# Performance work log

Measured on AMD Instinct MI355X. Metric: run time of the kernel, lower is better.

The kernel has to match this reference:

```python
import jax, jax.numpy as jnp
import numpy as np

N, K, C, G = 20000, 16, 256, 16
EPS = 1e-5


def _bn(x, p):
    # p: (4, C) stacked [gamma, beta, running_mean, running_var]; inference-mode BN
    g, b, m, v = p[0], p[1], p[2], p[3]
    return (x - m) * jax.lax.rsqrt(v + EPS) * g + b


def setup_inputs() -> dict:
    key = jax.random.key(0)
    ks = jax.random.split(key, 24)

    def w(k, shape):
        return jax.random.normal(k, shape, jnp.float32) * 0.02

    def bn_params(k, c):
        gamma = 1.0 + 0.02 * jax.random.normal(k, (c,), jnp.float32)
        return jnp.stack([gamma, jnp.zeros(c, jnp.float32), jnp.zeros(c, jnp.float32), jnp.ones(c, jnp.float32)])

    return {
        'feat': jax.random.normal(ks[0], (N, C), jnp.float32),
        'coord': jax.random.normal(ks[1], (N, 3), jnp.float32),
        'knn_indexes': jax.random.randint(ks[2], (N, K), 0, N),
        'Wq': w(ks[3], (C, C)), 'bq': w(ks[4], (C,)), 'bnq': bn_params(ks[5], C),
        'Wk': w(ks[6], (C, C)), 'bk': w(ks[7], (C,)), 'bnk': bn_params(ks[8], C),
        'Wv': w(ks[9], (C, C)), 'bv': w(ks[10], (C,)),
        'Wp1': w(ks[11], (3, C)), 'bp1': w(ks[12], (C,)), 'bnp': bn_params(ks[13], C),
        'Wp2': w(ks[14], (C, C)), 'bp2': w(ks[15], (C,)),
        'Ww1': w(ks[16], (C, G)), 'bw1': w(ks[17], (G,)), 'bnw': bn_params(ks[18], G),
        'Ww2': w(ks[19], (G, G)), 'bw2': w(ks[20], (G,)),
    }


def reference(feat, coord, knn_indexes, Wq, bq, bnq, Wk, bk, bnk, Wv, bv,
              Wp1, bp1, bnp, Wp2, bp2, Ww1, bw1, bnw, Ww2, bw2):
    # q/k: Linear -> BN -> ReLU ; v: Linear
    q = jax.nn.relu(_bn(feat @ Wq + bq, bnq))            # (n, c)
    k_all = jax.nn.relu(_bn(feat @ Wk + bk, bnk))        # (n, c)
    v_all = feat @ Wv + bv                               # (n, c)

    mask = jnp.sign(knn_indexes + 1).astype(feat.dtype)  # (n, k); -1 indices are padding
    safe_idx = jnp.clip(knn_indexes, 0, None)

    # kNN gather: padded entries map to zero rows in the torch code -> mask them here
    key_g = k_all[safe_idx] * mask[..., None]            # (n, k, c)
    value = v_all[safe_idx] * mask[..., None]            # (n, k, c)
    pos = (coord[safe_idx] - coord[:, None, :]) * mask[..., None]  # (n, k, 3)

    relation_qk = key_g - q[:, None, :]                  # (n, k, c)

    # positional-encoding bias MLP: Linear(3->c) -> BN -> ReLU -> Linear(c->c)
    peb = jax.nn.relu(_bn(pos @ Wp1 + bp1, bnp)) @ Wp2 + bp2  # (n, k, c)
    relation_qk = relation_qk + peb
    value = value + peb

    # weight encoding: Linear(c->g) -> BN -> ReLU -> Linear(g->g)
    weight = jax.nn.relu(_bn(relation_qk @ Ww1 + bw1, bnw)) @ Ww2 + bw2  # (n, k, g)
    weight = jax.nn.softmax(weight, axis=1) * mask[..., None]            # softmax over neighbors

    value = value.reshape(N, K, G, C // G)               # (n, k, g, i)
    out = jnp.einsum('nsgi,nsg->ngi', value, weight)     # group-wise weighted sum over neighbors
    return out.reshape(N, C)
```

## Files before the change

### kernel.cpp

```cpp
#include <hip/hip_runtime.h>
#include <hip/hip_bf16.h>

#define N_PTS 20000
#define KNN 16
#define C 256
#define G 16
#define EPS 1e-5f
#define NP 16

typedef __attribute__((ext_vector_type(8))) short short8;
typedef __attribute__((ext_vector_type(4))) short short4b;
typedef __attribute__((ext_vector_type(4))) float f32x4;

__device__ inline unsigned short f2bf(float f) {
    unsigned int x = __float_as_uint(f);
    unsigned int r = (x + 0x7fffu + ((x >> 16) & 1u)) >> 16;
    return (unsigned short)r;
}
__device__ inline float bf2f(unsigned int u) {
    return __uint_as_float((u & 0xffffu) << 16);
}
__device__ inline short f2bfs(float f) { return (short)f2bf(f); }

__global__ __launch_bounds__(256) void k_prep(const float* Wp2, const float* bp2,
                                              const float* Ww1, const float* bw1,
                                              float* w2w1, float* c1,
                                              unsigned short* wp2bft) {
    __shared__ float red[256][17];
    int t = threadIdx.x, b = blockIdx.x;
    float src = (b < C) ? Wp2[b * C + t] : bp2[t];
    #pragma unroll
    for (int g = 0; g < G; ++g) red[t][g] = src * Ww1[t * G + g];
    __syncthreads();
    for (int s = 128; s > 0; s >>= 1) {
        if (t < s) {
            #pragma unroll
            for (int g = 0; g < G; ++g) red[t][g] += red[t + s][g];
        }
        __syncthreads();
    }
    if (t < G) {
        if (b < C) w2w1[b * G + t] = red[0][t];
        else       c1[t] = red[0][t] + bw1[t];
    }
    if (b < C) wp2bft[t * C + b] = f2bf(Wp2[b * C + t]);
}

__global__ __launch_bounds__(512, 2) void k_qkv(
    const float* __restrict__ feat,
    const float* __restrict__ Wq, const float* __restrict__ bq, const float* __restrict__ bnq,
    const float* __restrict__ Wk, const float* __restrict__ bk, const float* __restrict__ bnk,
    const float* __restrict__ Wv, const float* __restrict__ bv,
    unsigned short* __restrict__ q_out, unsigned short* __restrict__ k_out,
    unsigned short* __restrict__ v_out) {
    __shared__ __align__(16) unsigned short Asl[128][40];
    __shared__ __align__(16) unsigned short Bsl[256][40];

    const int t = threadIdx.x;
    const int m0 = blockIdx.x * 128;
    const int z = blockIdx.z;
    const float* W    = (z == 0) ? Wq : (z == 1) ? Wk : Wv;
    const float* bias = (z == 0) ? bq : (z == 1) ? bk : bv;
    const float* bn   = (z == 0) ? bnq : bnk;

    const int wv = t >> 6, lane = t & 63, h = lane >> 4, ln = lane & 15;
    const int wm = wv >> 2, wn = wv & 3;

    f32x4 acc[4][4];
    #pragma unroll
    for (int i = 0; i < 4; ++i)
        #pragma unroll
        for (int j = 0; j < 4; ++j) acc[i][j] = (f32x4){0.f, 0.f, 0.f, 0.f};

    const int ar = t >> 3, ak = (t & 7) * 4;
    const int bk_n = (t & 63) * 4, bk_k = t >> 6;

    for (int kb = 0; kb < C; kb += 32) {
        #pragma unroll
        for (int ps = 0; ps < 2; ++ps) {
            int r = ar + 64 * ps;
            int gm = m0 + r; if (gm > N_PTS - 1) gm = N_PTS - 1;
            float4 f = *(const float4*)&feat[gm * C + kb + ak];
            unsigned int u0 = f2bf(f.x) | ((unsigned int)f2bf(f.y) << 16);
            unsigned int u1 = f2bf(f.z) | ((unsigned int)f2bf(f.w) << 16);
            *(uint2*)&Asl[r][ak] = make_uint2(u0, u1);
        }
        #pragma unroll
        for (int ps = 0; ps < 4; ++ps) {
            int kk = bk_k + 8 * ps;
            float4 w = *(const float4*)&W[(kb + kk) * C + bk_n];
            Bsl[bk_n + 0][kk] = f2bf(w.x);
            Bsl[bk_n + 1][kk] = f2bf(w.y);
            Bsl[bk_n + 2][kk] = f2bf(w.z);
            Bsl[bk_n + 3][kk] = f2bf(w.w);
        }
        __syncthreads();
        short8 af[4], bf[4];
        #pragma unroll
        for (int mf = 0; mf < 4; ++mf) af[mf] = *(const short8*)&Asl[64 * wm + 16 * mf + ln][8 * h];
        #pragma unroll
        for (int nf = 0; nf < 4; ++nf) bf[nf] = *(const short8*)&Bsl[64 * wn + 16 * nf + ln][8 * h];
        #pragma unroll
        for (int mf = 0; mf < 4; ++mf)
            #pragma unroll
            for (int nf = 0; nf < 4; ++nf)
                acc[mf][nf] = __builtin_amdgcn_mfma_f32_16x16x32_bf16(af[mf], bf[nf], acc[mf][nf], 0, 0, 0);
        __syncthreads();
    }

    unsigned short* dst = (z == 0) ? q_out : (z == 1) ? k_out : v_out;
    float scv[4], shv[4];
    int cidx[4];
    #pragma unroll
    for (int nf = 0; nf < 4; ++nf) {
        int c = 64 * wn + 16 * nf + ln;
        cidx[nf] = c;
        float bi = bias[c];
        if (z < 2) {
            float ga = bn[c], be = bn[C + c], mu = bn[2 * C + c], va = bn[3 * C + c];
            float s = ga * rsqrtf(va + EPS);
            scv[nf] = s; shv[nf] = (bi - mu) * s + be;
        } else { scv[nf] = 1.f; shv[nf] = bi; }
    }
    #pragma unroll
    for (int mf = 0; mf < 4; ++mf) {
        #pragma unroll
        for (int reg = 0; reg < 4; ++reg) {
            int m = m0 + 64 * wm + 16 * mf + 4 * h + reg;
            if (m >= N_PTS) continue;
            #pragma unroll
            for (int nf = 0; nf < 4; ++nf) {
                float x = acc[mf][nf][reg] * scv[nf] + shv[nf];
                if (z < 2) x = fmaxf(x, 0.f);
                dst[m * C + cidx[nf]] = f2bf(x);
            }
        }
    }
}

__global__ __launch_bounds__(256) void k_qkw(const unsigned short* q_ws, const unsigned short* k_ws,
                                             const float* Ww1, float* qw1, float* kw1) {
    __shared__ float tile[16][260];
    __shared__ float wT[G][260];
    int t = threadIdx.x;
    const unsigned short* src = blockIdx.y ? k_ws : q_ws;
    float* dst = blockIdx.y ? kw1 : qw1;
    int r0 = blockIdx.x * 16;
    #pragma unroll
    for (int i = 0; i < 16; ++i) {
        int e = t + 256 * i;
        wT[e & 15][e >> 4] = Ww1[e];
    }
    #pragma unroll
    for (int i = 0; i < 4; ++i) {
        int e4 = t + 256 * i;
        int row = e4 >> 6, col = (e4 & 63) * 4;
        uint2 u = *(const uint2*)&src[(r0 + row) * C + col];
        tile[row][col + 0] = bf2f(u.x);
        tile[row][col + 1] = bf2f(u.x >> 16);
        tile[row][col + 2] = bf2f(u.y);
        tile[row][col + 3] = bf2f(u.y >> 16);
    }
    __syncthreads();
    int r = t >> 4, g = t & 15;
    float acc = 0.f;
    for (int c = 0; c < C; c += 4) {
        float4 a = *(float4*)&tile[r][c];
        float4 w = *(float4*)&wT[g][c];
        acc += a.x * w.x + a.y * w.y + a.z * w.z + a.w * w.w;
    }
    dst[(r0 + r) * G + g] = acc;
}

__global__ __launch_bounds__(256, 2) void k_attn(
    const float* __restrict__ coord, const int* __restrict__ knn,
    const float* __restrict__ Wp1, const float* __restrict__ bp1, const float* __restrict__ bnp,
    const float* __restrict__ bp2,
    const float* __restrict__ Ww2, const float* __restrict__ bw2, const float* __restrict__ bnw,
    const float* __restrict__ w2w1, const float* __restrict__ c1,
    const float* __restrict__ qw1, const float* __restrict__ kw1,
    const unsigned short* __restrict__ vb, const unsigned short* __restrict__ wp2bft,
    float* __restrict__ out)
{
    __shared__ __align__(16) int   safe_s[256];
    __shared__ __align__(16) float wp1c[256][4];
    __shared__ __align__(16) unsigned short wt_l[16][16][20];
    __shared__ __align__(16) unsigned short hwbuf[10368];

    const int t = threadIdx.x;
    const int n0 = blockIdx.x * NP;
    const int wv = t >> 6, lane = t & 63, h = lane >> 4, ln = lane & 15;
    const short8 z8 = (short8){0, 0, 0, 0, 0, 0, 0, 0};

    float scwv, shwv, bw2v, c1v;
    {
        float ga = bnw[ln], be = bnw[G + ln], mu = bnw[2 * G + ln], va = bnw[3 * G + ln];
        scwv = ga * rsqrtf(va + EPS);
        shwv = be - mu * scwv;
        bw2v = bw2[ln];
        c1v  = c1[ln];
    }

    #pragma unroll
    for (int i = 0; i < 16; ++i) {
        int e = t + 256 * i;
        hwbuf[(e & 15) * 264 + (e >> 4)] = f2bf(w2w1[e]);
    }
    {
        float ga = bnp[t], be = bnp[C + t], mu = bnp[2 * C + t], va = bnp[3 * C + t];
        float s = ga * rsqrtf(va + EPS);
        wp1c[t][0] = Wp1[t] * s;
        wp1c[t][1] = Wp1[C + t] * s;
        wp1c[t][2] = Wp1[2 * C + t] * s;
        wp1c[t][3] = (bp1[t] - mu) * s + be;
        hwbuf[4224 + (t & 15) * 16 + (t >> 4)] = f2bf(Ww2[t]);
    }
    float px0, py0, pz0, mk0; int safe0;
    {
        const int n = n0 + (t >> 4);
        int ii = knn[n * KNN + (t & 15)];
        mk0 = (ii >= 0) ? 1.f : 0.f;
        safe0 = ii < 0 ? 0 : ii;
        safe_s[t] = safe0;
        px0 = (coord[safe0 * 3]     - coord[n * 3])     * mk0;
        py0 = (coord[safe0 * 3 + 1] - coord[n * 3 + 1]) * mk0;
        pz0 = (coord[safe0 * 3 + 2] - coord[n * 3 + 2]) * mk0;
    }
    __syncthreads();

    float prx[4], pry[4], prz[4];
    #pragma unroll
    for (int q = 0; q < 4; ++q) {
        int src = 16 * q + ln;
        prx[q] = __shfl(px0, src, 64);
        pry[q] = __shfl(py0, src, 64);
        prz[q] = __shfl(pz0, src, 64);
    }

    f32x4 accB[4];
    #pragma unroll
    for (int q = 0; q < 4; ++q) accB[q] = (f32x4){0.f, 0.f, 0.f, 0.f};
    for (int ks = 0; ks < 8; ++ks) {
        int d0 = ks * 32 + h * 8;
        short8 afr[4];
        #pragma unroll
        for (int hp = 0; hp < 2; ++hp) {
            float4 wpc[4];
            #pragma unroll
            for (int j = 0; j < 4; ++j) wpc[j] = *(const float4*)&wp1c[d0 + 4 * hp + j][0];
            #pragma unroll
            for (int q = 0; q < 4; ++q) {
                #pragma unroll
                for (int j = 0; j < 4; ++j) {
                    float hh = fmaxf(prx[q] * wpc[j].x + pry[q] * wpc[j].y + prz[q] * wpc[j].z + wpc[j].w, 0.f);
                    afr[q][4 * hp + j] = f2bfs(hh);
                }
            }
        }
        short8 bfr = *(const short8*)&hwbuf[ln * 264 + d0];
        #pragma unroll
        for (int q = 0; q < 4; ++q)
            accB[q] = __builtin_amdgcn_mfma_f32_16x16x32_bf16(afr[q], bfr, accB[q], 0, 0, 0);
    }

    #pragma unroll
    for (int q = 0; q < 4; ++q) {
        const int p = 4 * wv + q;
        float mkq[4]; int sfq[4];
        #pragma unroll
        for (int reg = 0; reg < 4; ++reg) {
            int src = 16 * q + 4 * h + reg;
            mkq[reg] = __shfl(mk0, src, 64);
            sfq[reg] = __shfl(safe0, src, 64);
        }
        #pragma unroll
        for (int reg = 0; reg < 4; ++reg) {
            float kv = kw1[sfq[reg] * G + ln];
            float qv = qw1[(n0 + p) * G + ln];
            float x = accB[q][reg] + kv * mkq[reg] - qv + c1v;
            float w1 = fmaxf(scwv * x + shwv, 0.f);
            hwbuf[4480 + wv * 384 + (4 * h + reg) * 24 + ln] = f2bf(w1);
        }
        short8 a = z8, b = z8;
        if (h < 2) {
            a = *(const short8*)&hwbuf[4480 + wv * 384 + ln * 24 + 8 * h];
            b = *(const short8*)&hwbuf[4224 + ln * 16 + 8 * h];
        }
        f32x4 w2v4 = __builtin_amdgcn_mfma_f32_16x16x32_bf16(
            a, b, (f32x4){bw2v, bw2v, bw2v, bw2v}, 0, 0, 0);
        float w2r[4] = {w2v4[0], w2v4[1], w2v4[2], w2v4[3]};
        float m = fmaxf(fmaxf(w2r[0], w2r[1]), fmaxf(w2r[2], w2r[3]));
        m = fmaxf(m, __shfl_xor(m, 16, 64));
        m = fmaxf(m, __shfl_xor(m, 32, 64));
        float e4[4], s = 0.f;
        #pragma unroll
        for (int reg = 0; reg < 4; ++reg) { e4[reg] = __expf(w2r[reg] - m); s += e4[reg]; }
        s += __shfl_xor(s, 16, 64);
        s += __shfl_xor(s, 32, 64);
        float inv = 1.f / s;
        float ws4 = 0.f;
        #pragma unroll
        for (int reg = 0; reg < 4; ++reg) {
            float wt = e4[reg] * inv * mkq[reg];
            ws4 += wt;
            wt_l[p][ln][4 * h + reg] = f2bf(wt);
        }
        ws4 += __shfl_xor(ws4, 16, 64);
        ws4 += __shfl_xor(ws4, 32, 64);
        if (h == 0) wt_l[p][ln][16] = f2bf(ws4);
    }

    __syncthreads();

    float pbx[4][4], pby[4][4], pbz[4][4];
    #pragma unroll
    for (int q = 0; q < 4; ++q) {
        #pragma unroll
        for (int j = 0; j < 4; ++j) {
            int src = 16 * q + 4 * h + j;
            pbx[q][j] = __shfl(px0, src, 64);
            pby[q][j] = __shfl(py0, src, 64);
            pbz[q][j] = __shfl(pz0, src, 64);
        }
    }
    short4b awt4[4];
    #pragma unroll
    for (int q = 0; q < 4; ++q)
        awt4[q] = *(const short4b*)&wt_l[4 * wv + q][ln][4 * h];

    const int gq = 4 * wv;
    f32x4 cacc[4];
    #pragma unroll
    for (int qq = 0; qq < 4; ++qq) cacc[qq] = (f32x4){0.f, 0.f, 0.f, 0.f};

    for (int ch = 0; ch < 16; ++ch) {
        const int bw = (ch & 1) * 5184;
        float4 wc = *(const float4*)&wp1c[ch * 16 + ln][0];
        #pragma unroll
        for (int q = 0; q < 4; ++q) {
            int p = 4 * wv + q;
            short4b bfr;
            #pragma unroll
            for (int j = 0; j < 4; ++j) {
                float hh = fmaxf(pbx[q][j] * wc.x + pby[q][j] * wc.y + pbz[q][j] * wc.z + wc.w, 0.f);
                bfr[j] = f2bfs(hh);
            }
            f32x4 hw = __builtin_amdgcn_mfma_f32_16x16x16bf16_1k(
                awt4[q], bfr, (f32x4){0.f, 0.f, 0.f, 0.f}, 0, 0, 0);
            #pragma unroll
            for (int reg = 0; reg < 4; ++reg)
                hwbuf[bw + (4 * h + reg) * 324 + p * 20 + ln] = f2bf(hw[reg]);
        }
        __syncthreads();
        const int dc = ch * 16;
        #pragma unroll
        for (int qq = 0; qq < 4; ++qq) {
            int g = gq + qq;
            short4b a = *(const short4b*)&hwbuf[bw + g * 324 + ln * 20 + 4 * h];
            short4b b = *(const short4b*)&wp2bft[(16 * g + ln) * C + dc + 4 * h];
            cacc[qq] = __builtin_amdgcn_mfma_f32_16x16x16bf16_1k(a, b, cacc[qq], 0, 0, 0);
        }
    }

    __syncthreads();
    float (*pebs)[256] = (float (*)[256])(void*)hwbuf;
    #pragma unroll
    for (int qq = 0; qq < 4; ++qq) {
        int g = gq + qq;
        #pragma unroll
        for (int reg = 0; reg < 4; ++reg) {
            int p = 4 * h + reg;
            pebs[p][16 * g + ln] = cacc[qq][reg];
        }
    }
    __syncthreads();

    {
        const int p_e = t >> 4, g_e = t & 15, c0 = g_e * 16;
        float o[16];
        #pragma unroll
        for (int j = 0; j < 16; ++j) o[j] = pebs[p_e][c0 + j];
        {
            float wsumv = bf2f(wt_l[p_e][g_e][16]);
            float4 b0 = *(const float4*)&bp2[c0];
            float4 b1 = *(const float4*)&bp2[c0 + 4];
            float4 b2 = *(const float4*)&bp2[c0 + 8];
            float4 b3 = *(const float4*)&bp2[c0 + 12];
            o[0] += wsumv * b0.x; o[1] += wsumv * b0.y; o[2] += wsumv * b0.z; o[3] += wsumv * b0.w;
            o[4] += wsumv * b1.x; o[5] += wsumv * b1.y; o[6] += wsumv * b1.z; o[7] += wsumv * b1.w;
            o[8] += wsumv * b2.x; o[9] += wsumv * b2.y; o[10] += wsumv * b2.z; o[11] += wsumv * b2.w;
            o[12] += wsumv * b3.x; o[13] += wsumv * b3.y; o[14] += wsumv * b3.z; o[15] += wsumv * b3.w;
        }
        #pragma unroll
        for (int k = 0; k < KNN; ++k) {
            int sf = safe_s[p_e * 16 + k];
            float w = bf2f(wt_l[p_e][g_e][k]);
            uint4 va = *(const uint4*)&vb[sf * C + c0];
            uint4 vc = *(const uint4*)&vb[sf * C + c0 + 8];
            o[0]  += w * bf2f(va.x); o[1]  += w * bf2f(va.x >> 16);
            o[2]  += w * bf2f(va.y); o[3]  += w * bf2f(va.y >> 16);
            o[4]  += w * bf2f(va.z); o[5]  += w * bf2f(va.z >> 16);
            o[6]  += w * bf2f(va.w); o[7]  += w * bf2f(va.w >> 16);
            o[8]  += w * bf2f(vc.x); o[9]  += w * bf2f(vc.x >> 16);
            o[10] += w * bf2f(vc.y); o[11] += w * bf2f(vc.y >> 16);
            o[12] += w * bf2f(vc.z); o[13] += w * bf2f(vc.z >> 16);
            o[14] += w * bf2f(vc.w); o[15] += w * bf2f(vc.w >> 16);
        }
        float* op = &out[(n0 + p_e) * C + c0];
        *(float4*)&op[0]  = make_float4(o[0], o[1], o[2], o[3]);
        *(float4*)&op[4]  = make_float4(o[4], o[5], o[6], o[7]);
        *(float4*)&op[8]  = make_float4(o[8], o[9], o[10], o[11]);
        *(float4*)&op[12] = make_float4(o[12], o[13], o[14], o[15]);
    }
}

extern "C" void kernel_launch(void* const* d_in, const int* in_sizes, int n_in,
                              void* d_out, int out_size, void* d_ws, size_t ws_size,
                              hipStream_t stream) {
    const float* feat  = (const float*)d_in[0];
    const float* coord = (const float*)d_in[1];
    const int*   knn   = (const int*)d_in[2];
    const float* Wq  = (const float*)d_in[3];
    const float* bq  = (const float*)d_in[4];
    const float* bnq = (const float*)d_in[5];
    const float* Wk  = (const float*)d_in[6];
    const float* bk  = (const float*)d_in[7];
    const float* bnk = (const float*)d_in[8];
    const float* Wv  = (const float*)d_in[9];
    const float* bv  = (const float*)d_in[10];
    const float* Wp1 = (const float*)d_in[11];
    const float* bp1 = (const float*)d_in[12];
    const float* bnp = (const float*)d_in[13];
    const float* Wp2 = (const float*)d_in[14];
    const float* bp2 = (const float*)d_in[15];
    const float* Ww1 = (const float*)d_in[16];
    const float* bw1 = (const float*)d_in[17];
    const float* bnw = (const float*)d_in[18];
    const float* Ww2 = (const float*)d_in[19];
    const float* bw2 = (const float*)d_in[20];

    float* ws = (float*)d_ws;
    unsigned short* q_ws = (unsigned short*)ws;
    unsigned short* k_ws = (unsigned short*)(ws + 2560000);
    unsigned short* v_ws = (unsigned short*)(ws + 5120000);
    float* qw1   = ws + 7680000;
    float* kw1   = ws + 8080000;
    float* w2w1  = ws + 8480000;
    float* c1    = ws + 8484096;
    unsigned short* wp2bft = (unsigned short*)(ws + 8500000);
    float* outp  = (float*)d_out;

    hipLaunchKernelGGL(k_prep, dim3(257), dim3(256), 0, stream,
                       Wp2, bp2, Ww1, bw1, w2w1, c1, wp2bft);
    hipLaunchKernelGGL(k_qkv, dim3(157, 1, 3), dim3(512), 0, stream,
                       feat, Wq, bq, bnq, Wk, bk, bnk, Wv, bv, q_ws, k_ws, v_ws);
    hipLaunchKernelGGL(k_qkw, dim3(1250, 2), dim3(256), 0, stream,
                       q_ws, k_ws, Ww1, qw1, kw1);
    hipLaunchKernelGGL(k_attn, dim3(1250), dim3(256), 0, stream,
                       coord, knn, Wp1, bp1, bnp, bp2, Ww2, bw2, bnw,
                       w2w1, c1, qw1, kw1, v_ws, wp2bft, outp);
}
```

Baseline: 161.0 us.

## Stage feat tile once in LDS and loop Q/K/V projections per block

```diff
diff --git a/kernel.cpp b/kernel.cpp
--- a/kernel.cpp
+++ b/kernel.cpp
@@ -13,9 +13,10 @@
 typedef __attribute__((ext_vector_type(4))) float f32x4;
 
 __device__ inline unsigned short f2bf(float f) {
-    unsigned int x = __float_as_uint(f);
-    unsigned int r = (x + 0x7fffu + ((x >> 16) & 1u)) >> 16;
-    return (unsigned short)r;
+    __hip_bfloat16 h = __float2bfloat16(f);
+    unsigned short u;
+    __builtin_memcpy(&u, &h, 2);
+    return u;
 }
 __device__ inline float bf2f(unsigned int u) {
     return __uint_as_float((u & 0xffffu) << 16);
@@ -53,86 +54,92 @@
     const float* __restrict__ Wv, const float* __restrict__ bv,
     unsigned short* __restrict__ q_out, unsigned short* __restrict__ k_out,
     unsigned short* __restrict__ v_out) {
-    __shared__ __align__(16) unsigned short Asl[128][40];
+    __shared__ __align__(16) unsigned short Af[64][264];
     __shared__ __align__(16) unsigned short Bsl[256][40];
 
     const int t = threadIdx.x;
-    const int m0 = blockIdx.x * 128;
-    const int z = blockIdx.z;
-    const float* W    = (z == 0) ? Wq : (z == 1) ? Wk : Wv;
-    const float* bias = (z == 0) ? bq : (z == 1) ? bk : bv;
-    const float* bn   = (z == 0) ? bnq : bnk;
-
-    const int wv = t >> 6, lane = t & 63, h = lane >> 4, ln = lane & 15;
-    const int wm = wv >> 2, wn = wv & 3;
-
-    f32x4 acc[4][4];
-    #pragma unroll
-    for (int i = 0; i < 4; ++i)
-        #pragma unroll
-        for (int j = 0; j < 4; ++j) acc[i][j] = (f32x4){0.f, 0.f, 0.f, 0.f};
-
-    const int ar = t >> 3, ak = (t & 7) * 4;
+    const int m0 = blockIdx.x * 64;
+    const int lane = t & 63, h = lane >> 4, ln = lane & 15;
+    const int wn = t >> 6;
+
+    {
+        int r = t >> 3;
+        int c0 = (t & 7) * 32;
+        int gm = m0 + r; if (gm > N_PTS - 1) gm = N_PTS - 1;
+        #pragma unroll
+        for (int i = 0; i < 8; ++i) {
+            float4 f = *(const float4*)&feat[gm * C + c0 + 4 * i];
+            Af[r][c0 + 4 * i + 0] = f2bf(f.x);
+            Af[r][c0 + 4 * i + 1] = f2bf(f.y);
+            Af[r][c0 + 4 * i + 2] = f2bf(f.z);
+            Af[r][c0 + 4 * i + 3] = f2bf(f.w);
+        }
+    }
+
     const int bk_n = (t & 63) * 4, bk_k = t >> 6;
 
-    for (int kb = 0; kb < C; kb += 32) {
-        #pragma unroll
-        for (int ps = 0; ps < 2; ++ps) {
-            int r = ar + 64 * ps;
-            int gm = m0 + r; if (gm > N_PTS - 1) gm = N_PTS - 1;
-            float4 f = *(const float4*)&feat[gm * C + kb + ak];
-            unsigned int u0 = f2bf(f.x) | ((unsigned int)f2bf(f.y) << 16);
-            unsigned int u1 = f2bf(f.z) | ((unsigned int)f2bf(f.w) << 16);
-            *(uint2*)&Asl[r][ak] = make_uint2(u0, u1);
-        }
-        #pragma unroll
-        for (int ps = 0; ps < 4; ++ps) {
-            int kk = bk_k + 8 * ps;
-            float4 w = *(const float4*)&W[(kb + kk) * C + bk_n];
-            Bsl[bk_n + 0][kk] = f2bf(w.x);
-            Bsl[bk_n + 1][kk] = f2bf(w.y);
-            Bsl[bk_n + 2][kk] = f2bf(w.z);
-            Bsl[bk_n + 3][kk] = f2bf(w.w);
-        }
-        __syncthreads();
-        short8 af[4], bf[4];
-        #pragma unroll
-        for (int mf = 0; mf < 4; ++mf) af[mf] = *(const short8*)&Asl[64 * wm + 16 * mf + ln][8 * h];
-        #pragma unroll
-        for (int nf = 0; nf < 4; ++nf) bf[nf] = *(const short8*)&Bsl[64 * wn + 16 * nf + ln][8 * h];
-        #pragma unroll
-        for (int mf = 0; mf < 4; ++mf)
-            #pragma unroll
-            for (int nf = 0; nf < 4; ++nf)
-                acc[mf][nf] = __builtin_amdgcn_mfma_f32_16x16x32_bf16(af[mf], bf[nf], acc[mf][nf], 0, 0, 0);
-        __syncthreads();
-    }
-
-    unsigned short* dst = (z == 0) ? q_out : (z == 1) ? k_out : v_out;
-    float scv[4], shv[4];
-    int cidx[4];
-    #pragma unroll
-    for (int nf = 0; nf < 4; ++nf) {
-        int c = 64 * wn + 16 * nf + ln;
-        cidx[nf] = c;
-        float bi = bias[c];
-        if (z < 2) {
-            float ga = bn[c], be = bn[C + c], mu = bn[2 * C + c], va = bn[3 * C + c];
-            float s = ga * rsqrtf(va + EPS);
-            scv[nf] = s; shv[nf] = (bi - mu) * s + be;
-        } else { scv[nf] = 1.f; shv[nf] = bi; }
-    }
-    #pragma unroll
-    for (int mf = 0; mf < 4; ++mf) {
-        #pragma unroll
-        for (int reg = 0; reg < 4; ++reg) {
-            int m = m0 + 64 * wm + 16 * mf + 4 * h + reg;
-            if (m >= N_PTS) continue;
-            #pragma unroll
-            for (int nf = 0; nf < 4; ++nf) {
-                float x = acc[mf][nf][reg] * scv[nf] + shv[nf];
-                if (z < 2) x = fmaxf(x, 0.f);
-                dst[m * C + cidx[nf]] = f2bf(x);
+    for (int z = 0; z < 3; ++z) {
+        const float* W    = (z == 0) ? Wq : (z == 1) ? Wk : Wv;
+        const float* bias = (z == 0) ? bq : (z == 1) ? bk : bv;
+        const float* bn   = (z == 0) ? bnq : bnk;
+
+        f32x4 acc[4][2];
+        #pragma unroll
+        for (int i = 0; i < 4; ++i) {
+            acc[i][0] = (f32x4){0.f, 0.f, 0.f, 0.f};
+            acc[i][1] = (f32x4){0.f, 0.f, 0.f, 0.f};
+        }
+
+        for (int kb = 0; kb < C; kb += 32) {
+            __syncthreads();
+            #pragma unroll
+            for (int ps = 0; ps < 4; ++ps) {
+                int kk = bk_k + 8 * ps;
+                float4 w = *(const float4*)&W[(kb + kk) * C + bk_n];
+                Bsl[bk_n + 0][kk] = f2bf(w.x);
+                Bsl[bk_n + 1][kk] = f2bf(w.y);
+                Bsl[bk_n + 2][kk] = f2bf(w.z);
+                Bsl[bk_n + 3][kk] = f2bf(w.w);
+            }
+            __syncthreads();
+            short8 af[4], bf[2];
+            #pragma unroll
+            for (int mf = 0; mf < 4; ++mf) af[mf] = *(const short8*)&Af[16 * mf + ln][kb + 8 * h];
+            #pragma unroll
+            for (int nf = 0; nf < 2; ++nf) bf[nf] = *(const short8*)&Bsl[32 * wn + 16 * nf + ln][8 * h];
+            #pragma unroll
+            for (int mf = 0; mf < 4; ++mf)
+                #pragma unroll
+                for (int nf = 0; nf < 2; ++nf)
+                    acc[mf][nf] = __builtin_amdgcn_mfma_f32_16x16x32_bf16(af[mf], bf[nf], acc[mf][nf], 0, 0, 0);
+        }
+
+        unsigned short* dst = (z == 0) ? q_out : (z == 1) ? k_out : v_out;
+        float scv[2], shv[2];
+        int cidx[2];
+        #pragma unroll
+        for (int nf = 0; nf < 2; ++nf) {
+            int c = 32 * wn + 16 * nf + ln;
+            cidx[nf] = c;
+            float bi = bias[c];
+            if (z < 2) {
+                float ga = bn[c], be = bn[C + c], mu = bn[2 * C + c], va = bn[3 * C + c];
+                float s = ga * rsqrtf(va + EPS);
+                scv[nf] = s; shv[nf] = (bi - mu) * s + be;
+            } else { scv[nf] = 1.f; shv[nf] = bi; }
+        }
+        #pragma unroll
+        for (int mf = 0; mf < 4; ++mf) {
+            #pragma unroll
+            for (int reg = 0; reg < 4; ++reg) {
+                int m = m0 + 16 * mf + 4 * h + reg;
+                if (m >= N_PTS) continue;
+                #pragma unroll
+                for (int nf = 0; nf < 2; ++nf) {
+                    float x = acc[mf][nf][reg] * scv[nf] + shv[nf];
+                    if (z < 2) x = fmaxf(x, 0.f);
+                    dst[m * C + cidx[nf]] = f2bf(x);
+                }
             }
         }
     }
@@ -452,7 +459,7 @@
 
     hipLaunchKernelGGL(k_prep, dim3(257), dim3(256), 0, stream,
                        Wp2, bp2, Ww1, bw1, w2w1, c1, wp2bft);
-    hipLaunchKernelGGL(k_qkv, dim3(157, 1, 3), dim3(512), 0, stream,
+    hipLaunchKernelGGL(k_qkv, dim3(313), dim3(512), 0, stream,
                        feat, Wq, bq, bnq, Wk, bk, bnk, Wv, bv, q_ws, k_ws, v_ws);
     hipLaunchKernelGGL(k_qkw, dim3(1250, 2), dim3(256), 0, stream,
                        q_ws, k_ws, Ww1, qw1, kw1);
```

After: 240.6 us. 49.4% more time.
